# Kernel tuning notes

Measured on AMD Instinct MI355X. Metric: run time of the kernel, lower is better.

The kernel has to match this reference:

```python
import jax, jax.numpy as jnp
import numpy as np

NUM_EXPERTS = 8
TOP_K = 2
HIDDEN = 1024
INTER = 4096  # ffn_hidden_size; fc1 produces 2*INTER for gated swiglu
TOKENS = 128


def setup_inputs() -> dict:
    key = jax.random.key(0)
    k1, k2, k3, k4 = jax.random.split(key, 4)
    hidden_states = jax.random.normal(k1, (TOKENS, HIDDEN), dtype=jnp.float32)
    routing = jax.random.normal(k2, (TOKENS, NUM_EXPERTS), dtype=jnp.float32)
    # fc1: [E, 2*inter, hidden] (rows 0:inter = up/linear path fed to act, inter:2*inter = gate)
    w1 = jax.random.normal(k3, (NUM_EXPERTS, 2 * INTER, HIDDEN), dtype=jnp.float32) * 0.02
    # fc2: [E, hidden, inter]
    w2 = jax.random.normal(k4, (NUM_EXPERTS, HIDDEN, INTER), dtype=jnp.float32) * 0.02
    return {"hidden_states": hidden_states, "routing": routing, "w1": w1, "w2": w2}


def reference(hidden_states, routing, w1, w2):
    # Top-k routing with renormalization (TRT-LLM RENORMALIZE mode):
    # softmax over all experts, take top-k probs, rescale to sum to 1.
    probs = jax.nn.softmax(routing, axis=-1)                  # [T, E]
    topv, topi = jax.lax.top_k(probs, TOP_K)                  # [T, k]
    scales = topv / jnp.sum(topv, axis=-1, keepdims=True)     # [T, k]

    num_experts = w1.shape[0]
    inter = w2.shape[2]
    out = jnp.zeros_like(hidden_states)
    # Fixed small loop over experts (structurally distinct weights); tokens stay vectorized.
    for e in range(num_experts):
        # combined routing coefficient of expert e for every token (0 if not selected)
        coef = jnp.sum(jnp.where(topi == e, scales, 0.0), axis=-1)   # [T]
        h = jnp.einsum('th,oh->to', hidden_states, w1[e])            # [T, 2*inter]
        act = jax.nn.silu(h[:, :inter]) * h[:, inter:]               # swiglu
        y = jnp.einsum('ti,hi->th', act, w2[e])                      # [T, hidden]
        out = out + coef[:, None] * y
    return out
```

## Files before the change

kernel.cpp:

```cpp
#include <hip/hip_runtime.h>
#include <hip/hip_bf16.h>

#define T_TOK 128
#define N_EXP 8
#define HID   1024
#define INTER 4096

typedef __bf16 bf16x8 __attribute__((ext_vector_type(8)));
typedef __bf16 bf16x4 __attribute__((ext_vector_type(4)));
typedef float  f32x4  __attribute__((ext_vector_type(4)));

__global__ void route_kernel(const float* __restrict__ routing,
                             int* __restrict__ cnt,
                             int* __restrict__ tok,
                             float* __restrict__ scal) {
    int t = threadIdx.x;
    int wave = t >> 6, lane = t & 63;

    float l[N_EXP];
#pragma unroll
    for (int e = 0; e < N_EXP; ++e) l[e] = routing[t * N_EXP + e];

    int i1 = 0; float v1 = l[0];
#pragma unroll
    for (int e = 1; e < N_EXP; ++e) if (l[e] > v1) { v1 = l[e]; i1 = e; }
    int i2 = -1; float v2 = -1e30f;
#pragma unroll
    for (int e = 0; e < N_EXP; ++e) if (e != i1 && l[e] > v2) { v2 = l[e]; i2 = e; }

    float s1 = 1.0f / (1.0f + __expf(v2 - v1));
    float s2 = 1.0f - s1;

    __shared__ unsigned long long wmask[2][N_EXP];
#pragma unroll
    for (int e = 0; e < N_EXP; ++e) {
        bool sel = (i1 == e) || (i2 == e);
        unsigned long long m = __ballot(sel);
        if (lane == 0) wmask[wave][e] = m;
    }
    __syncthreads();
#pragma unroll
    for (int e = 0; e < N_EXP; ++e) {
        bool sel = (i1 == e) || (i2 == e);
        unsigned long long m = __ballot(sel);
        int pre  = __popcll(m & ((1ull << lane) - 1ull));
        int base = (wave == 1) ? __popcll(wmask[0][e]) : 0;
        if (sel) {
            int slot = base + pre;
            tok [e * T_TOK + slot] = t;
            scal[e * T_TOK + slot] = (i1 == e) ? s1 : s2;
        }
        if (t == 0) cnt[e] = __popcll(wmask[0][e]) + __popcll(wmask[1][e]);
    }
}

__global__ void prep_kernel(const float* __restrict__ hidden,
                            const int* __restrict__ cnt,
                            const int* __restrict__ tok,
                            __bf16* __restrict__ abuf) {
    int b = blockIdx.x;
    int e = b >> 7, s = b & 127;
    if (s >= cnt[e]) return;
    int t = tok[e * T_TOK + s];
    const float4* src = (const float4*)(hidden + (size_t)t * HID);
    __bf16* dst = abuf + ((size_t)e * T_TOK + s) * HID;
#pragma unroll
    for (int it = 0; it < 4; ++it) {
        int idx = it * 64 + threadIdx.x;
        float4 v = src[idx];
        bf16x4 pk;
        pk[0] = (__bf16)v.x; pk[1] = (__bf16)v.y;
        pk[2] = (__bf16)v.z; pk[3] = (__bf16)v.w;
        *(bf16x4*)(dst + idx * 4) = pk;
    }
}

__device__ inline bf16x8 cvt8(float4 a, float4 b) {
    bf16x8 r;
    r[0] = (__bf16)a.x; r[1] = (__bf16)a.y; r[2] = (__bf16)a.z; r[3] = (__bf16)a.w;
    r[4] = (__bf16)b.x; r[5] = (__bf16)b.y; r[6] = (__bf16)b.z; r[7] = (__bf16)b.w;
    return r;
}

__global__ __launch_bounds__(256) void gemm1_kernel(
    const float* __restrict__ w1,
    const int* __restrict__ cnt,
    const __bf16* __restrict__ abuf,
    __bf16* __restrict__ act) {
    int bx = blockIdx.x;
    int e  = bx >> 6, nb = bx & 63;
    int wave = threadIdx.x >> 6, lane = threadIdx.x & 63;
    int n0 = nb * 64 + wave * 16;
    int c  = cnt[e];
    int mgs = (c + 15) >> 4;
    int lr = lane & 15;
    int lq = lane >> 4;

    const float* bl = w1 + ((size_t)e * 2 * INTER + n0 + lr) * HID + lq * 8;
    const float* bg = bl + (size_t)INTER * HID;
    const __bf16* ap = abuf + ((size_t)e * T_TOK + lr) * HID + lq * 8;

    f32x4 accl[8], accg[8];
#pragma unroll
    for (int m = 0; m < 8; ++m) {
        accl[m] = (f32x4){0.f, 0.f, 0.f, 0.f};
        accg[m] = (f32x4){0.f, 0.f, 0.f, 0.f};
    }

    for (int k0 = 0; k0 < HID; k0 += 32) {
        float4 fl0 = *(const float4*)(bl + k0);
        float4 fl1 = *(const float4*)(bl + k0 + 4);
        float4 fg0 = *(const float4*)(bg + k0);
        float4 fg1 = *(const float4*)(bg + k0 + 4);
        bf16x8 BL = cvt8(fl0, fl1);
        bf16x8 BG = cvt8(fg0, fg1);
#pragma unroll
        for (int m = 0; m < 8; ++m) {
            if (m < mgs) {
                bf16x8 A = *(const bf16x8*)(ap + (size_t)m * 16 * HID + k0);
                accl[m] = __builtin_amdgcn_mfma_f32_16x16x32_bf16(A, BL, accl[m], 0, 0, 0);
                accg[m] = __builtin_amdgcn_mfma_f32_16x16x32_bf16(A, BG, accg[m], 0, 0, 0);
            }
        }
    }

#pragma unroll
    for (int m = 0; m < 8; ++m) {
        if (m < mgs) {
#pragma unroll
            for (int r = 0; r < 4; ++r) {
                int slot = m * 16 + lq * 4 + r;
                if (slot < c) {
                    float lin  = accl[m][r];
                    float gate = accg[m][r];
                    float a = lin * (1.0f / (1.0f + __expf(-lin))) * gate;
                    act[((size_t)e * T_TOK + slot) * INTER + n0 + lr] = (__bf16)a;
                }
            }
        }
    }
}

__global__ __launch_bounds__(256) void gemm2_kernel(
    const float* __restrict__ w2,
    const int* __restrict__ cnt,
    const int* __restrict__ tok,
    const float* __restrict__ scal,
    const __bf16* __restrict__ act,
    float* __restrict__ out) {
    int bx = blockIdx.x;
    int ks = bx & 1, nb = (bx >> 1) & 15, e = bx >> 5;
    int wave = threadIdx.x >> 6, lane = threadIdx.x & 63;
    int n0 = nb * 64 + wave * 16;
    int c  = cnt[e];
    int mgs = (c + 15) >> 4;
    int lr = lane & 15, lq = lane >> 4;

    const float* bp = w2 + ((size_t)e * HID + n0 + lr) * INTER + ks * 2048 + lq * 8;
    const __bf16* ap = act + ((size_t)e * T_TOK + lr) * INTER + ks * 2048 + lq * 8;

    f32x4 acc[8];
#pragma unroll
    for (int m = 0; m < 8; ++m) acc[m] = (f32x4){0.f, 0.f, 0.f, 0.f};

    for (int k0 = 0; k0 < 2048; k0 += 32) {
        float4 f0 = *(const float4*)(bp + k0);
        float4 f1 = *(const float4*)(bp + k0 + 4);
        bf16x8 B = cvt8(f0, f1);
#pragma unroll
        for (int m = 0; m < 8; ++m) {
            if (m < mgs) {
                bf16x8 A = *(const bf16x8*)(ap + (size_t)m * 16 * INTER + k0);
                acc[m] = __builtin_amdgcn_mfma_f32_16x16x32_bf16(A, B, acc[m], 0, 0, 0);
            }
        }
    }

#pragma unroll
    for (int m = 0; m < 8; ++m) {
        if (m < mgs) {
#pragma unroll
            for (int r = 0; r < 4; ++r) {
                int slot = m * 16 + lq * 4 + r;
                if (slot < c) {
                    int   t    = tok [e * T_TOK + slot];
                    float coef = scal[e * T_TOK + slot];
                    atomicAdd(&out[(size_t)t * HID + n0 + lr], coef * acc[m][r]);
                }
            }
        }
    }
}

extern "C" void kernel_launch(void* const* d_in, const int* in_sizes, int n_in,
                              void* d_out, int out_size, void* d_ws, size_t ws_size,
                              hipStream_t stream) {
    const float* hidden  = (const float*)d_in[0];
    const float* routing = (const float*)d_in[1];
    const float* w1      = (const float*)d_in[2];
    const float* w2      = (const float*)d_in[3];
    float* out = (float*)d_out;

    char* ws = (char*)d_ws;
    int*    cnt  = (int*)ws;
    int*    tok  = (int*)(ws + 64);
    float*  scal = (float*)(ws + 64 + 4096);
    __bf16* abuf = (__bf16*)(ws + 16384);
    __bf16* act  = (__bf16*)(ws + 16384 + (size_t)2 * 1024 * 1024);

    hipMemsetAsync(d_out, 0, (size_t)out_size * sizeof(float), stream);

    route_kernel<<<1, 128, 0, stream>>>(routing, cnt, tok, scal);
    prep_kernel<<<N_EXP * T_TOK, 64, 0, stream>>>(hidden, cnt, tok, abuf);
    gemm1_kernel<<<N_EXP * 64, 256, 0, stream>>>(w1, cnt, abuf, act);
    gemm2_kernel<<<N_EXP * 32, 256, 0, stream>>>(w2, cnt, tok, scal, act, out);
}
```

Measured before the change: 545.2 us.

## Template MFMA loops on active M-groups and raise gemm2 split-K to four

Both GEMM inner loops are templated on the number of active 16-row token groups and selected through a switch. This removes per-iteration branches, lets A fragments be loaded ahead of the MFMAs, and unrolls by two. gemm2 now splits K four ways instead of two, doubling the block count so more of the GPU streams the fp32 weights in parallel, at the cost of more atomicAdd traffic on the output. Experts with no tokens now exit early.

New measurement: 483.2 us. -11.4%, faster.

```diff
diff --git a/kernel.cpp b/kernel.cpp
--- a/kernel.cpp
+++ b/kernel.cpp
@@ -75,11 +75,36 @@
     }
 }
 
-__device__ inline bf16x8 cvt8(float4 a, float4 b) {
+__device__ __forceinline__ bf16x8 cvt8(float4 a, float4 b) {
     bf16x8 r;
     r[0] = (__bf16)a.x; r[1] = (__bf16)a.y; r[2] = (__bf16)a.z; r[3] = (__bf16)a.w;
     r[4] = (__bf16)b.x; r[5] = (__bf16)b.y; r[6] = (__bf16)b.z; r[7] = (__bf16)b.w;
     return r;
+}
+
+template<int MG>
+__device__ __forceinline__ void g1_loop(const float* __restrict__ bl,
+                                        const float* __restrict__ bg,
+                                        const __bf16* __restrict__ ap,
+                                        f32x4* accl, f32x4* accg) {
+#pragma unroll 2
+    for (int k0 = 0; k0 < HID; k0 += 32) {
+        float4 fl0 = *(const float4*)(bl + k0);
+        float4 fl1 = *(const float4*)(bl + k0 + 4);
+        float4 fg0 = *(const float4*)(bg + k0);
+        float4 fg1 = *(const float4*)(bg + k0 + 4);
+        bf16x8 A[MG];
+#pragma unroll
+        for (int m = 0; m < MG; ++m)
+            A[m] = *(const bf16x8*)(ap + (size_t)m * 16 * HID + k0);
+        bf16x8 BL = cvt8(fl0, fl1);
+        bf16x8 BG = cvt8(fg0, fg1);
+#pragma unroll
+        for (int m = 0; m < MG; ++m) {
+            accl[m] = __builtin_amdgcn_mfma_f32_16x16x32_bf16(A[m], BL, accl[m], 0, 0, 0);
+            accg[m] = __builtin_amdgcn_mfma_f32_16x16x32_bf16(A[m], BG, accg[m], 0, 0, 0);
+        }
+    }
 }
 
 __global__ __launch_bounds__(256) void gemm1_kernel(
@@ -92,6 +117,7 @@
     int wave = threadIdx.x >> 6, lane = threadIdx.x & 63;
     int n0 = nb * 64 + wave * 16;
     int c  = cnt[e];
+    if (c == 0) return;
     int mgs = (c + 15) >> 4;
     int lr = lane & 15;
     int lq = lane >> 4;
@@ -107,26 +133,20 @@
         accg[m] = (f32x4){0.f, 0.f, 0.f, 0.f};
     }
 
-    for (int k0 = 0; k0 < HID; k0 += 32) {
-        float4 fl0 = *(const float4*)(bl + k0);
-        float4 fl1 = *(const float4*)(bl + k0 + 4);
-        float4 fg0 = *(const float4*)(bg + k0);
-        float4 fg1 = *(const float4*)(bg + k0 + 4);
-        bf16x8 BL = cvt8(fl0, fl1);
-        bf16x8 BG = cvt8(fg0, fg1);
-#pragma unroll
-        for (int m = 0; m < 8; ++m) {
-            if (m < mgs) {
-                bf16x8 A = *(const bf16x8*)(ap + (size_t)m * 16 * HID + k0);
-                accl[m] = __builtin_amdgcn_mfma_f32_16x16x32_bf16(A, BL, accl[m], 0, 0, 0);
-                accg[m] = __builtin_amdgcn_mfma_f32_16x16x32_bf16(A, BG, accg[m], 0, 0, 0);
-            }
-        }
+    switch (mgs) {
+        case 1: g1_loop<1>(bl, bg, ap, accl, accg); break;
+        case 2: g1_loop<2>(bl, bg, ap, accl, accg); break;
+        case 3: g1_loop<3>(bl, bg, ap, accl, accg); break;
+        case 4: g1_loop<4>(bl, bg, ap, accl, accg); break;
+        case 5: g1_loop<5>(bl, bg, ap, accl, accg); break;
+        case 6: g1_loop<6>(bl, bg, ap, accl, accg); break;
+        case 7: g1_loop<7>(bl, bg, ap, accl, accg); break;
+        default: g1_loop<8>(bl, bg, ap, accl, accg); break;
     }
 
 #pragma unroll
     for (int m = 0; m < 8; ++m) {
-        if (m < mgs) {
+        if (m * 16 < c) {
 #pragma unroll
             for (int r = 0; r < 4; ++r) {
                 int slot = m * 16 + lq * 4 + r;
@@ -141,6 +161,28 @@
     }
 }
 
+#define KSPLIT 4
+#define KCH (INTER / KSPLIT)
+
+template<int MG>
+__device__ __forceinline__ void g2_loop(const float* __restrict__ bp,
+                                        const __bf16* __restrict__ ap,
+                                        f32x4* acc) {
+#pragma unroll 2
+    for (int k0 = 0; k0 < KCH; k0 += 32) {
+        float4 f0 = *(const float4*)(bp + k0);
+        float4 f1 = *(const float4*)(bp + k0 + 4);
+        bf16x8 A[MG];
+#pragma unroll
+        for (int m = 0; m < MG; ++m)
+            A[m] = *(const bf16x8*)(ap + (size_t)m * 16 * INTER + k0);
+        bf16x8 B = cvt8(f0, f1);
+#pragma unroll
+        for (int m = 0; m < MG; ++m)
+            acc[m] = __builtin_amdgcn_mfma_f32_16x16x32_bf16(A[m], B, acc[m], 0, 0, 0);
+    }
+}
+
 __global__ __launch_bounds__(256) void gemm2_kernel(
     const float* __restrict__ w2,
     const int* __restrict__ cnt,
@@ -149,36 +191,35 @@
     const __bf16* __restrict__ act,
     float* __restrict__ out) {
     int bx = blockIdx.x;
-    int ks = bx & 1, nb = (bx >> 1) & 15, e = bx >> 5;
+    int ks = bx & (KSPLIT - 1), nb = (bx >> 2) & 15, e = bx >> 6;
     int wave = threadIdx.x >> 6, lane = threadIdx.x & 63;
     int n0 = nb * 64 + wave * 16;
     int c  = cnt[e];
+    if (c == 0) return;
     int mgs = (c + 15) >> 4;
     int lr = lane & 15, lq = lane >> 4;
 
-    const float* bp = w2 + ((size_t)e * HID + n0 + lr) * INTER + ks * 2048 + lq * 8;
-    const __bf16* ap = act + ((size_t)e * T_TOK + lr) * INTER + ks * 2048 + lq * 8;
+    const float* bp = w2 + ((size_t)e * HID + n0 + lr) * INTER + ks * KCH + lq * 8;
+    const __bf16* ap = act + ((size_t)e * T_TOK + lr) * INTER + ks * KCH + lq * 8;
 
     f32x4 acc[8];
 #pragma unroll
     for (int m = 0; m < 8; ++m) acc[m] = (f32x4){0.f, 0.f, 0.f, 0.f};
 
-    for (int k0 = 0; k0 < 2048; k0 += 32) {
-        float4 f0 = *(const float4*)(bp + k0);
-        float4 f1 = *(const float4*)(bp + k0 + 4);
-        bf16x8 B = cvt8(f0, f1);
-#pragma unroll
-        for (int m = 0; m < 8; ++m) {
-            if (m < mgs) {
-                bf16x8 A = *(const bf16x8*)(ap + (size_t)m * 16 * INTER + k0);
-                acc[m] = __builtin_amdgcn_mfma_f32_16x16x32_bf16(A, B, acc[m], 0, 0, 0);
-            }
-        }
+    switch (mgs) {
+        case 1: g2_loop<1>(bp, ap, acc); break;
+        case 2: g2_loop<2>(bp, ap, acc); break;
+        case 3: g2_loop<3>(bp, ap, acc); break;
+        case 4: g2_loop<4>(bp, ap, acc); break;
+        case 5: g2_loop<5>(bp, ap, acc); break;
+        case 6: g2_loop<6>(bp, ap, acc); break;
+        case 7: g2_loop<7>(bp, ap, acc); break;
+        default: g2_loop<8>(bp, ap, acc); break;
     }
 
 #pragma unroll
     for (int m = 0; m < 8; ++m) {
-        if (m < mgs) {
+        if (m * 16 < c) {
 #pragma unroll
             for (int r = 0; r < 4; ++r) {
                 int slot = m * 16 + lq * 4 + r;
@@ -213,5 +254,5 @@
     route_kernel<<<1, 128, 0, stream>>>(routing, cnt, tok, scal);
     prep_kernel<<<N_EXP * T_TOK, 64, 0, stream>>>(hidden, cnt, tok, abuf);
     gemm1_kernel<<<N_EXP * 64, 256, 0, stream>>>(w1, cnt, abuf, act);
-    gemm2_kernel<<<N_EXP * 32, 256, 0, stream>>>(w2, cnt, tok, scal, act, out);
-}
+    gemm2_kernel<<<N_EXP * 16 * KSPLIT, 256, 0, stream>>>(w2, cnt, tok, scal, act, out);
+}
```

## Split token groups across blocks, raise gemm2 K-split, unroll K loops

Applied to the files above, without the earlier changes.

Both GEMM kernels now split the token dimension into groups of 32 slots, each handled by its own block, with a template specialisation for one or two 16-row MFMA groups. gemm2's K split goes from 2 to 4. The K loops are unrolled by 4 so weight and activation loads are issued in batches ahead of the MFMAs. The aim is more blocks in flight and more memory-level parallelism on this weight-bandwidth-bound workload. The cost is that each fp32 weight tile is re-read by every token-group block, and gemm2 issues more atomics.

Result: slower. 651.9 us (+19.6%).

```diff
diff --git a/kernel.cpp b/kernel.cpp
--- a/kernel.cpp
+++ b/kernel.cpp
@@ -9,6 +9,8 @@
 typedef __bf16 bf16x8 __attribute__((ext_vector_type(8)));
 typedef __bf16 bf16x4 __attribute__((ext_vector_type(4)));
 typedef float  f32x4  __attribute__((ext_vector_type(4)));
+
+#define MFMA16(A, B, C) __builtin_amdgcn_mfma_f32_16x16x32_bf16(A, B, C, 0, 0, 0)
 
 __global__ void route_kernel(const float* __restrict__ routing,
                              int* __restrict__ cnt,
@@ -75,11 +77,68 @@
     }
 }
 
-__device__ inline bf16x8 cvt8(float4 a, float4 b) {
+__device__ __forceinline__ bf16x8 cvt8(float4 a, float4 b) {
     bf16x8 r;
     r[0] = (__bf16)a.x; r[1] = (__bf16)a.y; r[2] = (__bf16)a.z; r[3] = (__bf16)a.w;
     r[4] = (__bf16)b.x; r[5] = (__bf16)b.y; r[6] = (__bf16)b.z; r[7] = (__bf16)b.w;
     return r;
+}
+
+template<int MG>
+__device__ __forceinline__ void g1_body(const float* __restrict__ bl,
+                                        const float* __restrict__ bg,
+                                        const __bf16* __restrict__ ap,
+                                        __bf16* __restrict__ act,
+                                        int e, int n0, int lr, int lq,
+                                        int slot_base, int c) {
+    constexpr int UF = 4;
+    f32x4 accl[MG], accg[MG];
+#pragma unroll
+    for (int m = 0; m < MG; ++m) {
+        accl[m] = (f32x4){0.f, 0.f, 0.f, 0.f};
+        accg[m] = (f32x4){0.f, 0.f, 0.f, 0.f};
+    }
+
+    for (int k0 = 0; k0 < HID; k0 += 32 * UF) {
+        float4 WL[UF][2], WG[UF][2];
+        bf16x8 A[UF][MG];
+#pragma unroll
+        for (int u = 0; u < UF; ++u) {
+            WL[u][0] = *(const float4*)(bl + k0 + u * 32);
+            WL[u][1] = *(const float4*)(bl + k0 + u * 32 + 4);
+            WG[u][0] = *(const float4*)(bg + k0 + u * 32);
+            WG[u][1] = *(const float4*)(bg + k0 + u * 32 + 4);
+        }
+#pragma unroll
+        for (int u = 0; u < UF; ++u)
+#pragma unroll
+            for (int m = 0; m < MG; ++m)
+                A[u][m] = *(const bf16x8*)(ap + (size_t)m * 16 * HID + k0 + u * 32);
+#pragma unroll
+        for (int u = 0; u < UF; ++u) {
+            bf16x8 BL = cvt8(WL[u][0], WL[u][1]);
+            bf16x8 BG = cvt8(WG[u][0], WG[u][1]);
+#pragma unroll
+            for (int m = 0; m < MG; ++m) {
+                accl[m] = MFMA16(A[u][m], BL, accl[m]);
+                accg[m] = MFMA16(A[u][m], BG, accg[m]);
+            }
+        }
+    }
+
+#pragma unroll
+    for (int m = 0; m < MG; ++m) {
+#pragma unroll
+        for (int r = 0; r < 4; ++r) {
+            int slot = slot_base + m * 16 + lq * 4 + r;
+            if (slot < c) {
+                float lin  = accl[m][r];
+                float gate = accg[m][r];
+                float a = lin * (1.0f / (1.0f + __expf(-lin))) * gate;
+                act[((size_t)e * T_TOK + slot) * INTER + n0 + lr] = (__bf16)a;
+            }
+        }
+    }
 }
 
 __global__ __launch_bounds__(256) void gemm1_kernel(
@@ -87,55 +146,72 @@
     const int* __restrict__ cnt,
     const __bf16* __restrict__ abuf,
     __bf16* __restrict__ act) {
-    int bx = blockIdx.x;
-    int e  = bx >> 6, nb = bx & 63;
+    int bx  = blockIdx.x;
+    int mg2 = bx & 3, nb = (bx >> 2) & 63, e = bx >> 8;
+    int c   = cnt[e];
+    int rem = c - mg2 * 32;
+    if (rem <= 0) return;
+
     int wave = threadIdx.x >> 6, lane = threadIdx.x & 63;
     int n0 = nb * 64 + wave * 16;
-    int c  = cnt[e];
-    int mgs = (c + 15) >> 4;
-    int lr = lane & 15;
-    int lq = lane >> 4;
+    int lr = lane & 15, lq = lane >> 4;
+    int slot_base = mg2 * 32;
 
     const float* bl = w1 + ((size_t)e * 2 * INTER + n0 + lr) * HID + lq * 8;
     const float* bg = bl + (size_t)INTER * HID;
-    const __bf16* ap = abuf + ((size_t)e * T_TOK + lr) * HID + lq * 8;
-
-    f32x4 accl[8], accg[8];
-#pragma unroll
-    for (int m = 0; m < 8; ++m) {
-        accl[m] = (f32x4){0.f, 0.f, 0.f, 0.f};
-        accg[m] = (f32x4){0.f, 0.f, 0.f, 0.f};
-    }
-
-    for (int k0 = 0; k0 < HID; k0 += 32) {
-        float4 fl0 = *(const float4*)(bl + k0);
-        float4 fl1 = *(const float4*)(bl + k0 + 4);
-        float4 fg0 = *(const float4*)(bg + k0);
-        float4 fg1 = *(const float4*)(bg + k0 + 4);
-        bf16x8 BL = cvt8(fl0, fl1);
-        bf16x8 BG = cvt8(fg0, fg1);
-#pragma unroll
-        for (int m = 0; m < 8; ++m) {
-            if (m < mgs) {
-                bf16x8 A = *(const bf16x8*)(ap + (size_t)m * 16 * HID + k0);
-                accl[m] = __builtin_amdgcn_mfma_f32_16x16x32_bf16(A, BL, accl[m], 0, 0, 0);
-                accg[m] = __builtin_amdgcn_mfma_f32_16x16x32_bf16(A, BG, accg[m], 0, 0, 0);
-            }
-        }
-    }
-
-#pragma unroll
-    for (int m = 0; m < 8; ++m) {
-        if (m < mgs) {
-#pragma unroll
-            for (int r = 0; r < 4; ++r) {
-                int slot = m * 16 + lq * 4 + r;
-                if (slot < c) {
-                    float lin  = accl[m][r];
-                    float gate = accg[m][r];
-                    float a = lin * (1.0f / (1.0f + __expf(-lin))) * gate;
-                    act[((size_t)e * T_TOK + slot) * INTER + n0 + lr] = (__bf16)a;
-                }
+    const __bf16* ap = abuf + ((size_t)e * T_TOK + slot_base + lr) * HID + lq * 8;
+
+    if (rem > 16) g1_body<2>(bl, bg, ap, act, e, n0, lr, lq, slot_base, c);
+    else          g1_body<1>(bl, bg, ap, act, e, n0, lr, lq, slot_base, c);
+}
+
+#define KSPLIT 4
+#define KCH (INTER / KSPLIT)
+
+template<int MG>
+__device__ __forceinline__ void g2_body(const float* __restrict__ bp,
+                                        const __bf16* __restrict__ ap,
+                                        const int* __restrict__ tok,
+                                        const float* __restrict__ scal,
+                                        float* __restrict__ out,
+                                        int e, int n0, int lr, int lq,
+                                        int slot_base, int c) {
+    constexpr int UF = 4;
+    f32x4 acc[MG];
+#pragma unroll
+    for (int m = 0; m < MG; ++m) acc[m] = (f32x4){0.f, 0.f, 0.f, 0.f};
+
+    for (int k0 = 0; k0 < KCH; k0 += 32 * UF) {
+        float4 W[UF][2];
+        bf16x8 A[UF][MG];
+#pragma unroll
+        for (int u = 0; u < UF; ++u) {
+            W[u][0] = *(const float4*)(bp + k0 + u * 32);
+            W[u][1] = *(const float4*)(bp + k0 + u * 32 + 4);
+        }
+#pragma unroll
+        for (int u = 0; u < UF; ++u)
+#pragma unroll
+            for (int m = 0; m < MG; ++m)
+                A[u][m] = *(const bf16x8*)(ap + (size_t)m * 16 * INTER + k0 + u * 32);
+#pragma unroll
+        for (int u = 0; u < UF; ++u) {
+            bf16x8 B = cvt8(W[u][0], W[u][1]);
+#pragma unroll
+            for (int m = 0; m < MG; ++m)
+                acc[m] = MFMA16(A[u][m], B, acc[m]);
+        }
+    }
+
+#pragma unroll
+    for (int m = 0; m < MG; ++m) {
+#pragma unroll
+        for (int r = 0; r < 4; ++r) {
+            int slot = slot_base + m * 16 + lq * 4 + r;
+            if (slot < c) {
+                int   t    = tok [e * T_TOK + slot];
+                float coef = scal[e * T_TOK + slot];
+                atomicAdd(&out[(size_t)t * HID + n0 + lr], coef * acc[m][r]);
             }
         }
     }
@@ -148,48 +224,22 @@
     const float* __restrict__ scal,
     const __bf16* __restrict__ act,
     float* __restrict__ out) {
-    int bx = blockIdx.x;
-    int ks = bx & 1, nb = (bx >> 1) & 15, e = bx >> 5;
+    int bx  = blockIdx.x;
+    int mg2 = bx & 3, ks = (bx >> 2) & (KSPLIT - 1), nb = (bx >> 4) & 15, e = bx >> 8;
+    int c   = cnt[e];
+    int rem = c - mg2 * 32;
+    if (rem <= 0) return;
+
     int wave = threadIdx.x >> 6, lane = threadIdx.x & 63;
     int n0 = nb * 64 + wave * 16;
-    int c  = cnt[e];
-    int mgs = (c + 15) >> 4;
     int lr = lane & 15, lq = lane >> 4;
-
-    const float* bp = w2 + ((size_t)e * HID + n0 + lr) * INTER + ks * 2048 + lq * 8;
-    const __bf16* ap = act + ((size_t)e * T_TOK + lr) * INTER + ks * 2048 + lq * 8;
-
-    f32x4 acc[8];
-#pragma unroll
-    for (int m = 0; m < 8; ++m) acc[m] = (f32x4){0.f, 0.f, 0.f, 0.f};
-
-    for (int k0 = 0; k0 < 2048; k0 += 32) {
-        float4 f0 = *(const float4*)(bp + k0);
-        float4 f1 = *(const float4*)(bp + k0 + 4);
-        bf16x8 B = cvt8(f0, f1);
-#pragma unroll
-        for (int m = 0; m < 8; ++m) {
-            if (m < mgs) {
-                bf16x8 A = *(const bf16x8*)(ap + (size_t)m * 16 * INTER + k0);
-                acc[m] = __builtin_amdgcn_mfma_f32_16x16x32_bf16(A, B, acc[m], 0, 0, 0);
-            }
-        }
-    }
-
-#pragma unroll
-    for (int m = 0; m < 8; ++m) {
-        if (m < mgs) {
-#pragma unroll
-            for (int r = 0; r < 4; ++r) {
-                int slot = m * 16 + lq * 4 + r;
-                if (slot < c) {
-                    int   t    = tok [e * T_TOK + slot];
-                    float coef = scal[e * T_TOK + slot];
-                    atomicAdd(&out[(size_t)t * HID + n0 + lr], coef * acc[m][r]);
-                }
-            }
-        }
-    }
+    int slot_base = mg2 * 32;
+
+    const float* bp = w2 + ((size_t)e * HID + n0 + lr) * INTER + ks * KCH + lq * 8;
+    const __bf16* ap = act + ((size_t)e * T_TOK + slot_base + lr) * INTER + ks * KCH + lq * 8;
+
+    if (rem > 16) g2_body<2>(bp, ap, tok, scal, out, e, n0, lr, lq, slot_base, c);
+    else          g2_body<1>(bp, ap, tok, scal, out, e, n0, lr, lq, slot_base, c);
 }
 
 extern "C" void kernel_launch(void* const* d_in, const int* in_sizes, int n_in,
@@ -212,6 +262,6 @@
 
     route_kernel<<<1, 128, 0, stream>>>(routing, cnt, tok, scal);
     prep_kernel<<<N_EXP * T_TOK, 64, 0, stream>>>(hidden, cnt, tok, abuf);
-    gemm1_kernel<<<N_EXP * 64, 256, 0, stream>>>(w1, cnt, abuf, act);
-    gemm2_kernel<<<N_EXP * 32, 256, 0, stream>>>(w2, cnt, tok, scal, act, out);
-}
+    gemm1_kernel<<<N_EXP * 64 * 4, 256, 0, stream>>>(w1, cnt, abuf, act);
+    gemm2_kernel<<<N_EXP * 16 * KSPLIT * 4, 256, 0, stream>>>(w2, cnt, tok, scal, act, out);
+}
```
